# Kernel tuning notes

Hardware: AMD Instinct MI355X
Metric: run time of the kernel (lower is better)

Reference implementation:

```python
import jax, jax.numpy as jnp
import numpy as np

N_HEADS = 8
PROJ_DIM = 32


def _phi(x):
    # elu(x) + 1 feature map (always > 0)
    return jax.nn.elu(x) + 1.0


def _causal_linear(pq, pk, v):
    # Faithful to torch _linear_kernelized_attention masked branch:
    #   dpq_l = pq_l - pq_{l-1} (with pq_{-1}=0)
    #   result_l = cumsum_{m<=l} (dpq_m . v_m) * pk_m
    # The torch code materializes (N,H,L,D,D); here the identical math is
    # computed via a per-position scalar c_m = dpq_m . v_m, O(L*D) memory.
    dpq = pq - jnp.concatenate([jnp.zeros_like(pq[..., :1, :]), pq[..., :-1, :]], axis=-2)
    c = jnp.einsum('nhld,nhld->nhl', dpq, v)[..., None]  # (N,H,L,1)
    return jnp.cumsum(c * pk, axis=-2)  # (N,H,L,D)


def _bidir_linear(pq, pk, v):
    # Non-masked linear path: (pk^T v) first, then pq @ (.)
    right = jnp.einsum('nhld,nhle->nhde', pk, v)
    return jnp.einsum('nhqd,nhde->nhqe', pq, right)


def _attention(Y, X, Wq, Wk, Wv, mask):
    N, Lq, Dm = Y.shape
    Lk = X.shape[1]
    H, Pd = N_HEADS, PROJ_DIM
    # torch Linear: x @ W^T
    q = (Y @ Wq.T).reshape(N, Lq, H, Pd).transpose(0, 2, 1, 3)  # (N,H,Lq,Pd)
    k = (X @ Wk.T).reshape(N, Lk, H, Pd).transpose(0, 2, 1, 3)
    v = (X @ Wv.T).reshape(N, Lk, H, Pd).transpose(0, 2, 1, 3)
    pq, pk = _phi(q), _phi(k)
    fn = _causal_linear if mask else _bidir_linear
    num = fn(pq, pk, v)
    den = fn(pq, pk, jnp.ones_like(v))  # v_scale = ones expanded to D
    A = num / den
    return A.transpose(0, 2, 1, 3).reshape(N, Lq, H * Pd)


def setup_inputs() -> dict:
    key = jax.random.key(0)
    kY, kX, kq, kk, kv = jax.random.split(key, 5)
    N, L, dim = 2, 8192, N_HEADS * PROJ_DIM
    scale_in = 0.05            # keep phi(q),phi(k) ~ 1 so denominator stays positive
    scale_w = 1.0 / np.sqrt(dim)
    Y = scale_in * jax.random.normal(kY, (N, L, dim), dtype=jnp.float32)
    X = scale_in * jax.random.normal(kX, (N, L, dim), dtype=jnp.float32)
    Wq = scale_w * jax.random.normal(kq, (dim, dim), dtype=jnp.float32)
    Wk = scale_w * jax.random.normal(kk, (dim, dim), dtype=jnp.float32)
    Wv = scale_w * jax.random.normal(kv, (dim, dim), dtype=jnp.float32)
    return {"Y": Y, "X": X, "Wq": Wq, "Wk": Wk, "Wv": Wv, "mask": 1}


def reference(Y, X, Wq, Wk, Wv, mask):
    return _attention(Y, X, Wq, Wk, Wv, mask)
```

## Files before the change

### kernel.cpp

```cpp
#include <hip/hip_runtime.h>
#include <hip/hip_bf16.h>


typedef __attribute__((ext_vector_type(8))) short short8;
typedef __attribute__((ext_vector_type(4))) float f32x4;

__device__ __forceinline__ float phi_f(float x) {
    return x > 0.f ? x + 1.f : __expf(x);
}
__device__ __forceinline__ unsigned short f2bf(float x) {
    __hip_bfloat16 h = __float2bfloat16(x);
    return *reinterpret_cast<unsigned short*>(&h);
}
__device__ __forceinline__ float bf2f(unsigned short u) {
    return __uint_as_float(((unsigned int)u) << 16);
}

__global__ __launch_bounds__(256) void k_prepw(
        const float* __restrict__ Wq, const float* __restrict__ Wk,
        const float* __restrict__ Wv, unsigned short* __restrict__ Wf)
{
    const int g = blockIdx.x * 256 + threadIdx.x;
    const int mat = g >> 13, cc = g & 8191;
    const float* src = (mat == 0) ? Wq : (mat == 1 ? Wv : Wk);
    const int ln = cc & 15, qd = (cc >> 4) & 3, kt = (cc >> 6) & 7, jt = cc >> 9;
    const float* s = src + (size_t)(jt * 16 + ln) * 256 + kt * 32 + qd * 8;
    float4 f0 = *(const float4*)s, f1 = *(const float4*)(s + 4);
    short8 o;
    o[0] = f2bf(f0.x); o[1] = f2bf(f0.y); o[2] = f2bf(f0.z); o[3] = f2bf(f0.w);
    o[4] = f2bf(f1.x); o[5] = f2bf(f1.y); o[6] = f2bf(f1.z); o[7] = f2bf(f1.w);
    *(short8*)(Wf + (size_t)g * 8) = o;
}

#define LDA 280

__global__ __launch_bounds__(512, 4) void k_gemm(
        const float* __restrict__ Y, const float* __restrict__ X,
        const unsigned short* __restrict__ Wf,
        unsigned short* __restrict__ pk_out,
        float* __restrict__ c_out, float* __restrict__ cd_out,
        float* __restrict__ tot)
{
    __shared__ __align__(16) unsigned short Ys[33 * LDA];
    __shared__ __align__(16) unsigned short Xs[32 * LDA];
    __shared__ float scc[32][8], scd[32][8];
    __shared__ __align__(16) unsigned short spk[32 * 264];

    const int rb = blockIdx.x;
    const int n = rb >> 8, tile = rb & 255;
    const int mbase = rb * 32, lseg0 = tile * 32;
    const bool hasprev = (tile != 0);
    const int t = threadIdx.x, w = t >> 6, lane = t & 63;
    const int ln = lane & 15, qd = lane >> 4;

#pragma unroll
    for (int it = 0; it < 8; ++it) {
        const int idx = t + it * 512;
        const int half = idx >> 11, row = (idx >> 6) & 31, c4 = idx & 63;
        const float* s = (half ? X : Y) + (size_t)(mbase + row) * 256 + c4 * 4;
        float4 f = *(const float4*)s;
        ushort4 h4;
        h4.x = f2bf(f.x); h4.y = f2bf(f.y); h4.z = f2bf(f.z); h4.w = f2bf(f.w);
        unsigned short* dst = half ? Xs : Ys;
        *(ushort4*)&dst[row * LDA + c4 * 4] = h4;
    }
    if (t < 64) {
        const int prow = hasprev ? mbase - 1 : mbase;
        float4 f = *(const float4*)(Y + (size_t)prow * 256 + t * 4);
        ushort4 h4;
        h4.x = f2bf(f.x); h4.y = f2bf(f.y); h4.z = f2bf(f.z); h4.w = f2bf(f.w);
        *(ushort4*)&Ys[32 * LDA + t * 4] = h4;
    }
    __syncthreads();

    f32x4 aq[2][2], av[2][2], akk[2][2], aqp[2];
#pragma unroll
    for (int i = 0; i < 2; ++i)
#pragma unroll
        for (int j = 0; j < 2; ++j) {
            aq[i][j]  = (f32x4){0.f, 0.f, 0.f, 0.f};
            av[i][j]  = (f32x4){0.f, 0.f, 0.f, 0.f};
            akk[i][j] = (f32x4){0.f, 0.f, 0.f, 0.f};
        }
    aqp[0] = (f32x4){0.f, 0.f, 0.f, 0.f};
    aqp[1] = (f32x4){0.f, 0.f, 0.f, 0.f};
    const short8 z8 = {0, 0, 0, 0, 0, 0, 0, 0};
    const short8* W8 = (const short8*)Wf;

#pragma unroll
    for (int kt = 0; kt < 8; ++kt) {
        const int ko = kt * 32 + qd * 8;
        short8 ay0 = *(const short8*)&Ys[ln * LDA + ko];
        short8 ay1 = *(const short8*)&Ys[(16 + ln) * LDA + ko];
        short8 ax0 = *(const short8*)&Xs[ln * LDA + ko];
        short8 ax1 = *(const short8*)&Xs[(16 + ln) * LDA + ko];
        short8 ext = *(const short8*)&Ys[32 * LDA + ko];
        short8 ayp = (ln == 15) ? ext : z8;
#pragma unroll
        for (int jj = 0; jj < 2; ++jj) {
            const int jt = w * 2 + jj;
            short8 bq = W8[(((0 * 16 + jt) * 8 + kt) << 6) + lane];
            short8 bv = W8[(((1 * 16 + jt) * 8 + kt) << 6) + lane];
            short8 bk = W8[(((2 * 16 + jt) * 8 + kt) << 6) + lane];
            aq[0][jj]  = __builtin_amdgcn_mfma_f32_16x16x32_bf16(ay0, bq, aq[0][jj], 0, 0, 0);
            aq[1][jj]  = __builtin_amdgcn_mfma_f32_16x16x32_bf16(ay1, bq, aq[1][jj], 0, 0, 0);
            aqp[jj]    = __builtin_amdgcn_mfma_f32_16x16x32_bf16(ayp, bq, aqp[jj], 0, 0, 0);
            av[0][jj]  = __builtin_amdgcn_mfma_f32_16x16x32_bf16(ax0, bv, av[0][jj], 0, 0, 0);
            av[1][jj]  = __builtin_amdgcn_mfma_f32_16x16x32_bf16(ax1, bv, av[1][jj], 0, 0, 0);
            akk[0][jj] = __builtin_amdgcn_mfma_f32_16x16x32_bf16(ax0, bk, akk[0][jj], 0, 0, 0);
            akk[1][jj] = __builtin_amdgcn_mfma_f32_16x16x32_bf16(ax1, bk, akk[1][jj], 0, 0, 0);
        }
    }

#pragma unroll
    for (int i = 0; i < 2; ++i)
#pragma unroll
        for (int jj = 0; jj < 2; ++jj)
#pragma unroll
            for (int r = 0; r < 4; ++r) aq[i][jj][r] = phi_f(aq[i][jj][r]);
    float pprev[2];
#pragma unroll
    for (int jj = 0; jj < 2; ++jj) {
        float p15 = __shfl(aqp[jj][3], 48 + ln);
        pprev[jj] = hasprev ? phi_f(p15) : 0.f;
    }

    float cc_[2][4], cd_[2][4];
#pragma unroll
    for (int i = 0; i < 2; ++i)
#pragma unroll
        for (int r = 0; r < 4; ++r) { cc_[i][r] = 0.f; cd_[i][r] = 0.f; }
#pragma unroll
    for (int jj = 0; jj < 2; ++jj) {
        float carry = pprev[jj];
#pragma unroll
        for (int i = 0; i < 2; ++i) {
            const float p0 = aq[i][jj][0], p1 = aq[i][jj][1], p2 = aq[i][jj][2], p3 = aq[i][jj][3];
            const float up3 = __shfl_up(p3, 16);
            const float prev0 = (qd == 0) ? carry : up3;
            const float d0 = p0 - prev0, d1 = p1 - p0, d2 = p2 - p1, d3 = p3 - p2;
            cc_[i][0] += d0 * av[i][jj][0]; cd_[i][0] += d0;
            cc_[i][1] += d1 * av[i][jj][1]; cd_[i][1] += d1;
            cc_[i][2] += d2 * av[i][jj][2]; cd_[i][2] += d2;
            cc_[i][3] += d3 * av[i][jj][3]; cd_[i][3] += d3;
            carry = __shfl(p3, ln + 48);
        }
    }
#pragma unroll
    for (int i = 0; i < 2; ++i)
#pragma unroll
        for (int r = 0; r < 4; ++r) {
            float x = cc_[i][r];
            x += __shfl_xor(x, 1); x += __shfl_xor(x, 2);
            x += __shfl_xor(x, 4); x += __shfl_xor(x, 8);
            float y = cd_[i][r];
            y += __shfl_xor(y, 1); y += __shfl_xor(y, 2);
            y += __shfl_xor(y, 4); y += __shfl_xor(y, 8);
            if (ln == 0) {
                scc[i * 16 + qd * 4 + r][w] = x;
                scd[i * 16 + qd * 4 + r][w] = y;
            }
        }
    __syncthreads();
    {
        const int idx = t & 255, row = idx & 31, h = idx >> 5;
        const size_t gi = (size_t)(n * 8 + h) * 8192 + lseg0 + row;
        if (t < 256) c_out[gi]  = scc[row][h];
        else         cd_out[gi] = scd[row][h];
    }

#pragma unroll
    for (int i = 0; i < 2; ++i)
#pragma unroll
        for (int jj = 0; jj < 2; ++jj)
#pragma unroll
            for (int r = 0; r < 4; ++r) akk[i][jj][r] = phi_f(akk[i][jj][r]);
#pragma unroll
    for (int jj = 0; jj < 2; ++jj) {
        float tn = 0.f, td = 0.f;
#pragma unroll
        for (int i = 0; i < 2; ++i)
#pragma unroll
            for (int r = 0; r < 4; ++r) {
                const int row = i * 16 + qd * 4 + r;
                const float pv = akk[i][jj][r];
                tn += scc[row][w] * pv;
                td += scd[row][w] * pv;
            }
        tn += __shfl_xor(tn, 16); tn += __shfl_xor(tn, 32);
        td += __shfl_xor(td, 16); td += __shfl_xor(td, 32);
        if (qd == 0) {
            const int d = jj * 16 + ln;
            const size_t bi = ((size_t)(n * 8 + w) * 256 + tile) * 64;
            tot[bi + d]      = tn;
            tot[bi + 32 + d] = td;
        }
    }

#pragma unroll
    for (int i = 0; i < 2; ++i)
#pragma unroll
        for (int jj = 0; jj < 2; ++jj)
#pragma unroll
            for (int r = 0; r < 4; ++r)
                spk[(i * 16 + qd * 4 + r) * 264 + w * 32 + jj * 16 + ln] = f2bf(akk[i][jj][r]);
    __syncthreads();
#pragma unroll
    for (int it = 0; it < 2; ++it) {
        const int idx = t + 512 * it;
        const int row = idx >> 5, cg = idx & 31;
        short8 vals = *(const short8*)&spk[row * 264 + cg * 8];
        const int head = cg >> 2, d8 = (cg & 3) * 8;
        *(short8*)(pk_out + ((size_t)(n * 8 + head) * 8192 + lseg0 + row) * 32 + d8) = vals;
    }
}

__global__ __launch_bounds__(256) void k_scan(
        const unsigned short* __restrict__ pk, const float* __restrict__ c,
        const float* __restrict__ cd, const float* __restrict__ tot,
        float* __restrict__ out)
{
    __shared__ __align__(16) unsigned short spk[128 * 32];
    __shared__ float sc[128], sd[128];
    __shared__ float wsum[4][64], stile[4][64];

    const int bx = blockIdx.x, seg = bx >> 6, blk = bx & 63;
    const int n = seg >> 3, h = seg & 7;
    const int t = threadIdx.x, l0 = blk * 128;
    const int wv = t >> 6, lane = t & 63;
    const int T = blk * 4;

    const float* tb = tot + (size_t)seg * 256 * 64 + lane;
    float p0 = 0.f, p1 = 0.f, p2 = 0.f, p3 = 0.f,
          p4 = 0.f, p5 = 0.f, p6 = 0.f, p7 = 0.f;
    int i = wv;
    for (; i + 28 < T; i += 32) {
        p0 += tb[(i)      * 64]; p1 += tb[(i + 4)  * 64];
        p2 += tb[(i + 8)  * 64]; p3 += tb[(i + 12) * 64];
        p4 += tb[(i + 16) * 64]; p5 += tb[(i + 20) * 64];
        p6 += tb[(i + 24) * 64]; p7 += tb[(i + 28) * 64];
    }
    for (; i < T; i += 4) p0 += tb[i * 64];
    wsum[wv][lane]  = ((p0 + p1) + (p2 + p3)) + ((p4 + p5) + (p6 + p7));
    stile[wv][lane] = tb[(T + wv) * 64];

#pragma unroll
    for (int it = 0; it < 2; ++it) {
        const int idx = t + 256 * it;
        *(short8*)&spk[idx * 8] = *(const short8*)(pk + ((size_t)seg * 8192 + l0) * 32 + idx * 8);
    }
    if (t < 128) sc[t] = c[(size_t)seg * 8192 + l0 + t];
    else         sd[t - 128] = cd[(size_t)seg * 8192 + l0 + (t - 128)];
    __syncthreads();

    if (t < 128) {
        const int g = t >> 5, d = t & 31;
        float rn  = (wsum[0][d] + wsum[1][d]) + (wsum[2][d] + wsum[3][d]);
        float rd_ = (wsum[0][32 + d] + wsum[1][32 + d]) + (wsum[2][32 + d] + wsum[3][32 + d]);
#pragma unroll
        for (int i2 = 0; i2 < 3; ++i2)
            if (i2 < g) { rn += stile[i2][d]; rd_ += stile[i2][32 + d]; }
        float* ob = out + ((size_t)n * 8192 + l0 + g * 32) * 256 + h * 32 + d;
#pragma unroll
        for (int p = 0; p < 32; ++p) {
            const int m = g * 32 + p;
            const float pkv = bf2f(spk[m * 32 + d]);
            rn  += sc[m] * pkv;
            rd_ += sd[m] * pkv;
            ob[(size_t)p * 256] = rn / rd_;
        }
    }
}

extern "C" void kernel_launch(void* const* d_in, const int* in_sizes, int n_in,
                              void* d_out, int out_size, void* d_ws, size_t ws_size,
                              hipStream_t stream)
{
    const float* Y  = (const float*)d_in[0];
    const float* X  = (const float*)d_in[1];
    const float* Wq = (const float*)d_in[2];
    const float* Wk = (const float*)d_in[3];
    const float* Wv = (const float*)d_in[4];
    float* out = (float*)d_out;

    float* ws = (float*)d_ws;
    unsigned short* Wf = (unsigned short*)ws;
    unsigned short* pk = (unsigned short*)(ws + 98304);
    float* c   = ws + 98304 + 2097152;
    float* cd  = c  + 131072;
    float* tot = cd + 131072;

    hipLaunchKernelGGL(k_prepw, dim3(96),   dim3(256), 0, stream, Wq, Wk, Wv, Wf);
    hipLaunchKernelGGL(k_gemm,  dim3(512),  dim3(512), 0, stream,
                       Y, X, Wf, pk, c, cd, tot);
    hipLaunchKernelGGL(k_scan,  dim3(1024), dim3(256), 0, stream, pk, c, cd, tot, out);
}
```

Measured before the change: 110.5 us.

## Stage projection weights through double-buffered LDS via async global_load_lds

The GEMM kernel previously read the pre-swizzled bf16 weight fragments straight from global memory inside the MFMA loop. They are now streamed slice by slice (per k-tile and matrix) into a two-slot LDS buffer with global_load_lds, two slices ahead, using explicit waitcnt and barriers around each phase. The pk staging array aliases the new buffer. Nontemporal loads and stores are also applied to input reads and output writes. This adds 32KB of LDS per block and many extra block barriers, which may reduce occupancy and serialize waves.

```diff
diff --git a/kernel.cpp b/kernel.cpp
--- a/kernel.cpp
+++ b/kernel.cpp
@@ -14,6 +14,11 @@
 }
 __device__ __forceinline__ float bf2f(unsigned short u) {
     return __uint_as_float(((unsigned int)u) << 16);
+}
+__device__ __forceinline__ void glds16(const void* g, void* l) {
+    __builtin_amdgcn_global_load_lds(
+        (const __attribute__((address_space(1))) unsigned int*)g,
+        (__attribute__((address_space(3))) unsigned int*)l, 16, 0, 0);
 }
 
 __global__ __launch_bounds__(256) void k_prepw(
@@ -25,10 +30,11 @@
     const float* src = (mat == 0) ? Wq : (mat == 1 ? Wv : Wk);
     const int ln = cc & 15, qd = (cc >> 4) & 3, kt = (cc >> 6) & 7, jt = cc >> 9;
     const float* s = src + (size_t)(jt * 16 + ln) * 256 + kt * 32 + qd * 8;
-    float4 f0 = *(const float4*)s, f1 = *(const float4*)(s + 4);
+    f32x4 f0 = __builtin_nontemporal_load((const f32x4*)s);
+    f32x4 f1 = __builtin_nontemporal_load((const f32x4*)(s + 4));
     short8 o;
-    o[0] = f2bf(f0.x); o[1] = f2bf(f0.y); o[2] = f2bf(f0.z); o[3] = f2bf(f0.w);
-    o[4] = f2bf(f1.x); o[5] = f2bf(f1.y); o[6] = f2bf(f1.z); o[7] = f2bf(f1.w);
+    o[0] = f2bf(f0[0]); o[1] = f2bf(f0[1]); o[2] = f2bf(f0[2]); o[3] = f2bf(f0[3]);
+    o[4] = f2bf(f1[0]); o[5] = f2bf(f1[1]); o[6] = f2bf(f1[2]); o[7] = f2bf(f1[3]);
     *(short8*)(Wf + (size_t)g * 8) = o;
 }
 
@@ -44,7 +50,8 @@
     __shared__ __align__(16) unsigned short Ys[33 * LDA];
     __shared__ __align__(16) unsigned short Xs[32 * LDA];
     __shared__ float scc[32][8], scd[32][8];
-    __shared__ __align__(16) unsigned short spk[32 * 264];
+    __shared__ __align__(16) unsigned char WfB[2][16384];
+    unsigned short* spk = (unsigned short*)&WfB[0][0];
 
     const int rb = blockIdx.x;
     const int n = rb >> 8, tile = rb & 255;
@@ -53,25 +60,45 @@
     const int t = threadIdx.x, w = t >> 6, lane = t & 63;
     const int ln = lane & 15, qd = lane >> 4;
 
+    auto issue_slice = [&](int s) {
+        const int kt2 = s / 3, mat2 = s - kt2 * 3, b = s & 1;
+#pragma unroll
+        for (int it = 0; it < 2; ++it) {
+            const int idx = t + it * 512;
+            const int jt2 = idx >> 6, l2 = idx & 63;
+            const unsigned short* src =
+                Wf + (size_t)((((mat2 * 16 + jt2) * 8 + kt2) << 6) + l2) * 8;
+            glds16(src, &WfB[b][(w << 10) + (it << 13)]);
+        }
+    };
+
 #pragma unroll
     for (int it = 0; it < 8; ++it) {
         const int idx = t + it * 512;
         const int half = idx >> 11, row = (idx >> 6) & 31, c4 = idx & 63;
         const float* s = (half ? X : Y) + (size_t)(mbase + row) * 256 + c4 * 4;
-        float4 f = *(const float4*)s;
+        f32x4 f = __builtin_nontemporal_load((const f32x4*)s);
         ushort4 h4;
-        h4.x = f2bf(f.x); h4.y = f2bf(f.y); h4.z = f2bf(f.z); h4.w = f2bf(f.w);
+        h4.x = f2bf(f[0]); h4.y = f2bf(f[1]); h4.z = f2bf(f[2]); h4.w = f2bf(f[3]);
         unsigned short* dst = half ? Xs : Ys;
         *(ushort4*)&dst[row * LDA + c4 * 4] = h4;
     }
     if (t < 64) {
         const int prow = hasprev ? mbase - 1 : mbase;
-        float4 f = *(const float4*)(Y + (size_t)prow * 256 + t * 4);
+        f32x4 f = __builtin_nontemporal_load((const f32x4*)(Y + (size_t)prow * 256 + t * 4));
         ushort4 h4;
-        h4.x = f2bf(f.x); h4.y = f2bf(f.y); h4.z = f2bf(f.z); h4.w = f2bf(f.w);
+        h4.x = f2bf(f[0]); h4.y = f2bf(f[1]); h4.z = f2bf(f[2]); h4.w = f2bf(f[3]);
         *(ushort4*)&Ys[32 * LDA + t * 4] = h4;
     }
-    __syncthreads();
+
+    issue_slice(0);
+    __builtin_amdgcn_sched_barrier(0);
+    issue_slice(1);
+    __builtin_amdgcn_sched_barrier(0);
+    asm volatile("s_waitcnt lgkmcnt(0)" ::: "memory");
+    __builtin_amdgcn_sched_barrier(0);
+    __builtin_amdgcn_s_barrier();
+    __builtin_amdgcn_sched_barrier(0);
 
     f32x4 aq[2][2], av[2][2], akk[2][2], aqp[2];
 #pragma unroll
@@ -85,7 +112,24 @@
     aqp[0] = (f32x4){0.f, 0.f, 0.f, 0.f};
     aqp[1] = (f32x4){0.f, 0.f, 0.f, 0.f};
     const short8 z8 = {0, 0, 0, 0, 0, 0, 0, 0};
-    const short8* W8 = (const short8*)Wf;
+
+#define PH_OPEN(s)                                                      \
+    {                                                                   \
+        if ((s) == 0 || (s) >= 23)                                      \
+            asm volatile("s_waitcnt vmcnt(0)" ::: "memory");            \
+        else                                                            \
+            asm volatile("s_waitcnt vmcnt(2)" ::: "memory");            \
+        __builtin_amdgcn_sched_barrier(0);                              \
+        __builtin_amdgcn_s_barrier();                                   \
+        __builtin_amdgcn_sched_barrier(0);                              \
+    }
+#define PH_CLOSE(s)                                                     \
+    {                                                                   \
+        __builtin_amdgcn_s_barrier();                                   \
+        __builtin_amdgcn_sched_barrier(0);                              \
+        if ((s) + 2 < 24) issue_slice((s) + 2);                         \
+        __builtin_amdgcn_sched_barrier(0);                              \
+    }
 
 #pragma unroll
     for (int kt = 0; kt < 8; ++kt) {
@@ -96,21 +140,46 @@
         short8 ax1 = *(const short8*)&Xs[(16 + ln) * LDA + ko];
         short8 ext = *(const short8*)&Ys[32 * LDA + ko];
         short8 ayp = (ln == 15) ? ext : z8;
-#pragma unroll
-        for (int jj = 0; jj < 2; ++jj) {
-            const int jt = w * 2 + jj;
-            short8 bq = W8[(((0 * 16 + jt) * 8 + kt) << 6) + lane];
-            short8 bv = W8[(((1 * 16 + jt) * 8 + kt) << 6) + lane];
-            short8 bk = W8[(((2 * 16 + jt) * 8 + kt) << 6) + lane];
-            aq[0][jj]  = __builtin_amdgcn_mfma_f32_16x16x32_bf16(ay0, bq, aq[0][jj], 0, 0, 0);
-            aq[1][jj]  = __builtin_amdgcn_mfma_f32_16x16x32_bf16(ay1, bq, aq[1][jj], 0, 0, 0);
-            aqp[jj]    = __builtin_amdgcn_mfma_f32_16x16x32_bf16(ayp, bq, aqp[jj], 0, 0, 0);
-            av[0][jj]  = __builtin_amdgcn_mfma_f32_16x16x32_bf16(ax0, bv, av[0][jj], 0, 0, 0);
-            av[1][jj]  = __builtin_amdgcn_mfma_f32_16x16x32_bf16(ax1, bv, av[1][jj], 0, 0, 0);
-            akk[0][jj] = __builtin_amdgcn_mfma_f32_16x16x32_bf16(ax0, bk, akk[0][jj], 0, 0, 0);
-            akk[1][jj] = __builtin_amdgcn_mfma_f32_16x16x32_bf16(ax1, bk, akk[1][jj], 0, 0, 0);
-        }
-    }
+
+        const int s0 = kt * 3;
+        PH_OPEN(s0);
+        {
+            const unsigned short* bb = (const unsigned short*)&WfB[s0 & 1][0];
+            short8 b0 = *(const short8*)(bb + (w * 2 + 0) * 512 + lane * 8);
+            short8 b1 = *(const short8*)(bb + (w * 2 + 1) * 512 + lane * 8);
+            aq[0][0] = __builtin_amdgcn_mfma_f32_16x16x32_bf16(ay0, b0, aq[0][0], 0, 0, 0);
+            aq[1][0] = __builtin_amdgcn_mfma_f32_16x16x32_bf16(ay1, b0, aq[1][0], 0, 0, 0);
+            aqp[0]   = __builtin_amdgcn_mfma_f32_16x16x32_bf16(ayp, b0, aqp[0], 0, 0, 0);
+            aq[0][1] = __builtin_amdgcn_mfma_f32_16x16x32_bf16(ay0, b1, aq[0][1], 0, 0, 0);
+            aq[1][1] = __builtin_amdgcn_mfma_f32_16x16x32_bf16(ay1, b1, aq[1][1], 0, 0, 0);
+            aqp[1]   = __builtin_amdgcn_mfma_f32_16x16x32_bf16(ayp, b1, aqp[1], 0, 0, 0);
+        }
+        PH_CLOSE(s0);
+        PH_OPEN(s0 + 1);
+        {
+            const unsigned short* bb = (const unsigned short*)&WfB[(s0 + 1) & 1][0];
+            short8 b0 = *(const short8*)(bb + (w * 2 + 0) * 512 + lane * 8);
+            short8 b1 = *(const short8*)(bb + (w * 2 + 1) * 512 + lane * 8);
+            av[0][0] = __builtin_amdgcn_mfma_f32_16x16x32_bf16(ax0, b0, av[0][0], 0, 0, 0);
+            av[1][0] = __builtin_amdgcn_mfma_f32_16x16x32_bf16(ax1, b0, av[1][0], 0, 0, 0);
+            av[0][1] = __builtin_amdgcn_mfma_f32_16x16x32_bf16(ax0, b1, av[0][1], 0, 0, 0);
+            av[1][1] = __builtin_amdgcn_mfma_f32_16x16x32_bf16(ax1, b1, av[1][1], 0, 0, 0);
+        }
+        PH_CLOSE(s0 + 1);
+        PH_OPEN(s0 + 2);
+        {
+            const unsigned short* bb = (const unsigned short*)&WfB[(s0 + 2) & 1][0];
+            short8 b0 = *(const short8*)(bb + (w * 2 + 0) * 512 + lane * 8);
+            short8 b1 = *(const short8*)(bb + (w * 2 + 1) * 512 + lane * 8);
+            akk[0][0] = __builtin_amdgcn_mfma_f32_16x16x32_bf16(ax0, b0, akk[0][0], 0, 0, 0);
+            akk[1][0] = __builtin_amdgcn_mfma_f32_16x16x32_bf16(ax1, b0, akk[1][0], 0, 0, 0);
+            akk[0][1] = __builtin_amdgcn_mfma_f32_16x16x32_bf16(ax0, b1, akk[0][1], 0, 0, 0);
+            akk[1][1] = __builtin_amdgcn_mfma_f32_16x16x32_bf16(ax1, b1, akk[1][1], 0, 0, 0);
+        }
+        PH_CLOSE(s0 + 2);
+    }
+#undef PH_OPEN
+#undef PH_CLOSE
 
 #pragma unroll
     for (int i = 0; i < 2; ++i)
@@ -267,7 +336,7 @@
             const float pkv = bf2f(spk[m * 32 + d]);
             rn  += sc[m] * pkv;
             rd_ += sd[m] * pkv;
-            ob[(size_t)p * 256] = rn / rd_;
+            __builtin_nontemporal_store(rn / rd_, &ob[(size_t)p * 256]);
         }
     }
 }
```

Result: slower. 114.2 us (+3.3%).
